# Optimization experiments

Hardware: AMD Instinct MI355X
Metric: run time of the kernel (lower is better)

## Reference

```python
import jax, jax.numpy as jnp
import numpy as np

NUM_HEADS = 16
EMBED_DIM = 1024
SEQ_LEN = 2048
BATCH = 2


def setup_inputs() -> dict:
    key = jax.random.key(0)
    ks = jax.random.split(key, 7)
    E = EMBED_DIM
    scale = 1.0 / np.sqrt(E)
    return {
        "query": jax.random.normal(ks[0], (SEQ_LEN, BATCH, E), jnp.float32),
        "key": jax.random.normal(ks[1], (SEQ_LEN, BATCH, E), jnp.float32),
        "value": jax.random.normal(ks[2], (SEQ_LEN, BATCH, E), jnp.float32),
        "in_proj_weight": jax.random.normal(ks[3], (3 * E, E), jnp.float32) * scale,
        "in_proj_bias": jnp.zeros((3 * E,), jnp.float32),
        "out_proj_weight": jax.random.normal(ks[4], (E, E), jnp.float32) * scale,
        "out_proj_bias": jnp.zeros((E,), jnp.float32),
    }


def reference(query, key, value, in_proj_weight, in_proj_bias, out_proj_weight, out_proj_bias):
    T, B, E = query.shape
    H = NUM_HEADS
    d = E // H
    scaling = float(d) ** -0.5
    # in-projections: rows [0:E) -> q, [E:2E) -> k, [2E:3E) -> v
    q = query @ in_proj_weight[:E].T + in_proj_bias[:E]
    k = key @ in_proj_weight[E:2 * E].T + in_proj_bias[E:2 * E]
    v = value @ in_proj_weight[2 * E:].T + in_proj_bias[2 * E:]
    q = q * scaling
    # (T, B, E) -> (B*H, T, d)
    q = q.reshape(T, B * H, d).transpose(1, 0, 2)
    k = k.reshape(T, B * H, d).transpose(1, 0, 2)
    v = v.reshape(T, B * H, d).transpose(1, 0, 2)
    S = k.shape[1]
    scores = jnp.einsum('ntd,nsd->nts', q, k)  # (B*H, T, S)
    attn = jax.nn.softmax(scores, axis=-1)
    out = jnp.einsum('nts,nsd->ntd', attn, v)  # (B*H, T, d)
    out = out.transpose(1, 0, 2).reshape(T, B, E)
    out = out @ out_proj_weight.T + out_proj_bias
    attn_avg = attn.reshape(B, H, T, S).sum(axis=1) / H
    return out, attn_avg
```

## Files before the change

kernel.cpp:

```cpp
#include <hip/hip_runtime.h>
#include <math.h>

#define T_LEN 2048
#define BATCH 2
#define EMB 1024
#define NHEAD 16
#define HDIM 64
#define BH (BATCH*NHEAD)
#define MROWS (T_LEN*BATCH)
#define QSCALE (0.125f * 1.4426950408889634f)
#define HEADBUF ((size_t)BH*T_LEN*HDIM)

typedef __attribute__((ext_vector_type(8))) short bf16x8;
typedef __attribute__((ext_vector_type(4))) float f32x4;

#define MFMA16(a,b,c) __builtin_amdgcn_mfma_f32_16x16x32_bf16(a,b,c,0,0,0)

__device__ __forceinline__ short f2bf(float f) {
    union { float f; unsigned u; } v; v.f = f;
    unsigned r = (v.u + 0x7FFFu + ((v.u >> 16) & 1u)) >> 16;
    return (short)(unsigned short)r;
}
__device__ __forceinline__ float bf2f(short s) {
    union { unsigned u; float f; } v; v.u = ((unsigned)(unsigned short)s) << 16;
    return v.f;
}
__device__ __forceinline__ unsigned cvtpk(float a, float b) {
    unsigned r;
    asm("v_cvt_pk_bf16_f32 %0, %1, %2" : "=v"(r) : "v"(a), "v"(b));
    return r;
}
__device__ __forceinline__ void gload16(const void* g, void* l) {
    __builtin_amdgcn_global_load_lds(
        (const __attribute__((address_space(1))) unsigned*)g,
        (__attribute__((address_space(3))) unsigned*)l, 16, 0, 0);
}

__global__ __launch_bounds__(256) void tobf16_kernel(
    const float* __restrict__ q, const float* __restrict__ k,
    const float* __restrict__ v, const float* __restrict__ w,
    const float* __restrict__ wo, short* __restrict__ out)
{
    size_t i8 = ((size_t)blockIdx.x * 256 + threadIdx.x) * 8;
    const float* src; size_t off;
    if (i8 < 12582912) {
        int sel = (int)(i8 >> 22);
        src = (sel == 0) ? q : (sel == 1) ? k : v;
        off = i8 & 4194303;
    } else if (i8 < 15728640) {
        src = w;  off = i8 - 12582912;
    } else {
        src = wo; off = i8 - 15728640;
    }
    float4 f0 = *(const float4*)(src + off);
    float4 f1 = *(const float4*)(src + off + 4);
    bf16x8 o;
    o[0]=f2bf(f0.x); o[1]=f2bf(f0.y); o[2]=f2bf(f0.z); o[3]=f2bf(f0.w);
    o[4]=f2bf(f1.x); o[5]=f2bf(f1.y); o[6]=f2bf(f1.z); o[7]=f2bf(f1.w);
    *(bf16x8*)(out + i8) = o;
}

__global__ __launch_bounds__(256) void inproj_gemm(
    const short* __restrict__ Xq, const short* __restrict__ Xk,
    const short* __restrict__ Xv, const short* __restrict__ Wb,
    const float* __restrict__ bias,
    short* __restrict__ qbuf, short* __restrict__ kbuf, short* __restrict__ vbuf)
{
    const int mBase = blockIdx.x * 128;
    const int nBase = blockIdx.y * 128;
    const int which = nBase >> 10;
    const short* __restrict__ X = (which == 0) ? Xq : (which == 1) ? Xk : Xv;
    short* __restrict__ dst = (which == 0) ? qbuf : (which == 1) ? kbuf : vbuf;

    __shared__ short Ast[128][64];
    __shared__ short Bst[128][64];

    const int tid  = threadIdx.x;
    const int lane = tid & 63;
    const int w    = tid >> 6;
    const int wr   = w >> 1, wc = w & 1;
    const int lr   = lane & 15, lg = lane >> 4;
    const int srow = tid >> 3;
    const int scol = (tid & 7) * 8;

    f32x4 acc[4][4] = {};

    for (int kb = 0; kb < EMB; kb += 64) {
        __syncthreads();
        #pragma unroll
        for (int j = 0; j < 4; ++j) {
            gload16(X  + (size_t)(mBase + j * 32 + srow) * EMB + kb + scol,
                    (char*)Ast + j * 4096 + w * 1024);
            gload16(Wb + (size_t)(nBase + j * 32 + srow) * EMB + kb + scol,
                    (char*)Bst + j * 4096 + w * 1024);
        }
        __syncthreads();
        #pragma unroll
        for (int ks = 0; ks < 2; ++ks) {
            bf16x8 af[4], bfr[4];
            #pragma unroll
            for (int rg = 0; rg < 4; ++rg)
                af[rg] = *(const bf16x8*)&Ast[wr * 64 + rg * 16 + lr][ks * 32 + lg * 8];
            #pragma unroll
            for (int cg = 0; cg < 4; ++cg)
                bfr[cg] = *(const bf16x8*)&Bst[wc * 64 + cg * 16 + lr][ks * 32 + lg * 8];
            #pragma unroll
            for (int rg = 0; rg < 4; ++rg)
                #pragma unroll
                for (int cg = 0; cg < 4; ++cg)
                    acc[rg][cg] = MFMA16(af[rg], bfr[cg], acc[rg][cg]);
        }
    }

    #pragma unroll
    for (int rg = 0; rg < 4; ++rg) {
        #pragma unroll
        for (int cg = 0; cg < 4; ++cg) {
            int n  = nBase + wc * 64 + cg * 16 + lr;
            int e  = n & 1023;
            int h  = e >> 6, dd = e & 63;
            float bs = bias[n];
            #pragma unroll
            for (int ri = 0; ri < 4; ++ri) {
                int m = mBase + wr * 64 + rg * 16 + lg * 4 + ri;
                int t = m >> 1, b = m & 1;
                float val = acc[rg][cg][ri] + bs;
                if (which == 0) val *= QSCALE;
                dst[((size_t)(b * NHEAD + h) * T_LEN + t) * HDIM + dd] = f2bf(val);
            }
        }
    }
}

__global__ __launch_bounds__(256) void flash_kernel(
    const short* __restrict__ qb, const short* __restrict__ kbuf,
    const short* __restrict__ vbuf, short* __restrict__ h1,
    short* __restrict__ h2, float* __restrict__ mlws)
{
    const int qt = blockIdx.x;
    const int hb = blockIdx.y;

    __shared__ short Kst[64][64];
    __shared__ short VT [64][64];
    __shared__ short Pst[64][72];

    const int tid  = threadIdx.x;
    const int lane = tid & 63;
    const int w    = tid >> 6;
    const int lr   = lane & 15, lg = lane >> 4;

    bf16x8 qa0, qa1;
    {
        const short* qsrc = qb + ((size_t)hb * T_LEN + qt * 64 + w * 16 + lr) * HDIM;
        qa0 = *(const bf16x8*)(qsrc + lg * 8);
        qa1 = *(const bf16x8*)(qsrc + 32 + lg * 8);
    }
    const int krow  = (lane >> 3);
    const int kc16  = (lane & 7) ^ krow;
    const int rb0 = ((0 + lg) ^ (lr & 7)) * 16;
    const int rb1 = ((4 + lg) ^ (lr & 7)) * 16;

    float m_r = -INFINITY, l_r = 0.f;
    f32x4 o_acc[4] = {};

    for (int st = 0; st < T_LEN / 64; ++st) {
        __syncthreads();
        #pragma unroll
        for (int it = 0; it < 2; ++it) {
            int r = (w * 2 + it) * 8 + krow;
            gload16(kbuf + ((size_t)hb * T_LEN + st * 64 + r) * HDIM + kc16 * 8,
                    (char*)Kst + (w * 2 + it) * 1024);
        }
        {
            int dc = tid & 7, s0 = (tid >> 3) * 2;
            const short* v0 = vbuf + ((size_t)hb * T_LEN + st * 64 + s0) * HDIM + dc * 8;
            bf16x8 va  = *(const bf16x8*)v0;
            bf16x8 vb2 = *(const bf16x8*)(v0 + HDIM);
            #pragma unroll
            for (int j = 0; j < 8; ++j) {
                int d = dc * 8 + j;
                unsigned pk = ((unsigned)(unsigned short)va[j]) |
                              (((unsigned)(unsigned short)vb2[j]) << 16);
                int byte = (d << 7) + (s0 << 1);
                byte ^= (((d & 7) ^ (d >> 3)) << 4);
                *(unsigned*)((char*)VT + byte) = pk;
            }
        }
        __syncthreads();

        f32x4 sc[4] = {};
        #pragma unroll
        for (int sg = 0; sg < 4; ++sg) {
            const char* krowp = (const char*)Kst + (sg * 16 + lr) * 128;
            bf16x8 kf0 = *(const bf16x8*)(krowp + rb0);
            bf16x8 kf1 = *(const bf16x8*)(krowp + rb1);
            sc[sg] = MFMA16(kf0, qa0, sc[sg]);
            sc[sg] = MFMA16(kf1, qa1, sc[sg]);
        }

        float mx = sc[0][0];
        #pragma unroll
        for (int sg = 0; sg < 4; ++sg)
            #pragma unroll
            for (int ri = 0; ri < 4; ++ri)
                mx = fmaxf(mx, sc[sg][ri]);
        mx = fmaxf(mx, __shfl_xor(mx, 16));
        mx = fmaxf(mx, __shfl_xor(mx, 32));
        if (__any(mx - m_r > 8.0f)) {
            float mnew = fmaxf(m_r, mx);
            float scl  = exp2f(m_r - mnew);
            l_r *= scl;
            m_r = mnew;
            float sclq[4];
            #pragma unroll
            for (int ri = 0; ri < 4; ++ri) sclq[ri] = __shfl(scl, lg * 20 + ri);
            #pragma unroll
            for (int dsub = 0; dsub < 4; ++dsub)
                #pragma unroll
                for (int ri = 0; ri < 4; ++ri)
                    o_acc[dsub][ri] *= sclq[ri];
        }
        float p[4][4], psum = 0.f;
        #pragma unroll
        for (int sg = 0; sg < 4; ++sg)
            #pragma unroll
            for (int ri = 0; ri < 4; ++ri) {
                p[sg][ri] = exp2f(sc[sg][ri] - m_r);
                psum += p[sg][ri];
            }
        psum += __shfl_xor(psum, 16);
        psum += __shfl_xor(psum, 32);
        l_r += psum;

        #pragma unroll
        for (int sg = 0; sg < 4; ++sg) {
            uint2 pk;
            pk.x = cvtpk(p[sg][0], p[sg][1]);
            pk.y = cvtpk(p[sg][2], p[sg][3]);
            *(uint2*)&Pst[w * 16 + lr][sg * 16 + lg * 4] = pk;
        }

        #pragma unroll
        for (int ks = 0; ks < 2; ++ks) {
            bf16x8 pa = *(const bf16x8*)&Pst[w * 16 + lr][ks * 32 + lg * 8];
            #pragma unroll
            for (int dsub = 0; dsub < 4; ++dsub) {
                int d = dsub * 16 + lr;
                int byte = (d << 7) + ((ks * 32 + lg * 8) << 1);
                byte ^= (((d & 7) ^ (d >> 3)) << 4);
                bf16x8 vf = *(const bf16x8*)((char*)VT + byte);
                o_acc[dsub] = MFMA16(pa, vf, o_acc[dsub]);
            }
        }
    }

    float inv = 1.0f / l_r;
    float invq[4];
    #pragma unroll
    for (int ri = 0; ri < 4; ++ri) invq[ri] = __shfl(inv, lg * 20 + ri);
    #pragma unroll
    for (int ri = 0; ri < 4; ++ri) {
        int row = qt * 64 + w * 16 + lg * 4 + ri;
        #pragma unroll
        for (int dsub = 0; dsub < 4; ++dsub) {
            float x = o_acc[dsub][ri] * invq[ri];
            size_t idx = ((size_t)hb * T_LEN + row) * HDIM + dsub * 16 + lr;
            short a = f2bf(x);
            h1[idx] = a;
            h2[idx] = f2bf(x - bf2f(a));
        }
    }
    if (lg == 0) {
        int row = qt * 64 + w * 16 + lr;
        mlws[(size_t)hb * T_LEN + row] = m_r + __log2f(l_r);
    }
}

__global__ __launch_bounds__(256) void avg_kernel(
    const short* __restrict__ qbuf, const short* __restrict__ kbuf,
    const float* __restrict__ mlws, float* __restrict__ attn_avg)
{
    const int st = blockIdx.x;
    const int qt = blockIdx.y;
    const int b  = blockIdx.z;

    __shared__ short K4[4][64][64];

    const int tid  = threadIdx.x;
    const int lane = tid & 63;
    const int w    = tid >> 6;
    const int lr   = lane & 15, lg = lane >> 4;

    f32x4 acc[4] = {};

    for (int rnd = 0; rnd < 4; ++rnd) {
        __syncthreads();
        #pragma unroll
        for (int hh = 0; hh < 4; ++hh) {
            int hb = b * NHEAD + rnd * 4 + hh;
            #pragma unroll
            for (int j = 0; j < 2; ++j) {
                int row = j * 32 + (tid >> 3);
                int col = (tid & 7) * 8;
                gload16(kbuf + ((size_t)hb * T_LEN + st * 64 + row) * HDIM + col,
                        (char*)K4[hh] + j * 4096 + w * 1024);
            }
        }
        __syncthreads();
        #pragma unroll
        for (int hh = 0; hh < 4; ++hh) {
            int hb = b * NHEAD + rnd * 4 + hh;
            const short* qsrc = qbuf + ((size_t)hb * T_LEN + qt * 64 + w * 16 + lr) * HDIM;
            bf16x8 qa0 = *(const bf16x8*)(qsrc + lg * 8);
            bf16x8 qa1 = *(const bf16x8*)(qsrc + 32 + lg * 8);

            f32x4 sc[4] = {};
            #pragma unroll
            for (int sg = 0; sg < 4; ++sg) {
                bf16x8 kf0 = *(const bf16x8*)&K4[hh][sg * 16 + lr][lg * 8];
                bf16x8 kf1 = *(const bf16x8*)&K4[hh][sg * 16 + lr][32 + lg * 8];
                sc[sg] = MFMA16(qa0, kf0, sc[sg]);
                sc[sg] = MFMA16(qa1, kf1, sc[sg]);
            }

            #pragma unroll
            for (int ri = 0; ri < 4; ++ri) {
                int row = qt * 64 + w * 16 + lg * 4 + ri;
                float ml = mlws[(size_t)hb * T_LEN + row];
                #pragma unroll
                for (int sg = 0; sg < 4; ++sg)
                    acc[sg][ri] += exp2f(sc[sg][ri] - ml);
            }
        }
    }

    const float invH = 1.0f / (float)NHEAD;
    #pragma unroll
    for (int ri = 0; ri < 4; ++ri) {
        int row = qt * 64 + w * 16 + lg * 4 + ri;
        #pragma unroll
        for (int sg = 0; sg < 4; ++sg)
            attn_avg[((size_t)b * T_LEN + row) * T_LEN + st * 64 + sg * 16 + lr] =
                acc[sg][ri] * invH;
    }
}

__global__ __launch_bounds__(256) void outproj_gemm(
    const short* __restrict__ h1, const short* __restrict__ h2,
    const short* __restrict__ Wob, const float* __restrict__ bo,
    float* __restrict__ out)
{
    const int mBase = blockIdx.x * 128;
    const int nBase = blockIdx.y * 128;

    __shared__ short A1st[128][64];
    __shared__ short A2st[128][64];
    __shared__ short Bst [128][64];

    const int tid  = threadIdx.x;
    const int lane = tid & 63;
    const int w    = tid >> 6;
    const int wr   = w >> 1, wc = w & 1;
    const int lr   = lane & 15, lg = lane >> 4;
    const int srow = tid >> 3;
    const int scol = (tid & 7) * 8;

    f32x4 acc[4][4] = {};

    for (int kb = 0; kb < EMB; kb += 64) {
        const int h = kb >> 6;
        __syncthreads();
        #pragma unroll
        for (int j = 0; j < 4; ++j) {
            int m = mBase + j * 32 + srow;
            int t = m >> 1, b = m & 1;
            size_t aoff = ((size_t)(b * NHEAD + h) * T_LEN + t) * HDIM + scol;
            gload16(h1 + aoff, (char*)A1st + j * 4096 + w * 1024);
            gload16(h2 + aoff, (char*)A2st + j * 4096 + w * 1024);
            gload16(Wob + (size_t)(nBase + j * 32 + srow) * EMB + kb + scol,
                    (char*)Bst + j * 4096 + w * 1024);
        }
        __syncthreads();
        #pragma unroll
        for (int ks = 0; ks < 2; ++ks) {
            bf16x8 a1[4], a2[4], bfr[4];
            #pragma unroll
            for (int rg = 0; rg < 4; ++rg) {
                a1[rg] = *(const bf16x8*)&A1st[wr * 64 + rg * 16 + lr][ks * 32 + lg * 8];
                a2[rg] = *(const bf16x8*)&A2st[wr * 64 + rg * 16 + lr][ks * 32 + lg * 8];
            }
            #pragma unroll
            for (int cg = 0; cg < 4; ++cg)
                bfr[cg] = *(const bf16x8*)&Bst[wc * 64 + cg * 16 + lr][ks * 32 + lg * 8];
            #pragma unroll
            for (int rg = 0; rg < 4; ++rg)
                #pragma unroll
                for (int cg = 0; cg < 4; ++cg) {
                    acc[rg][cg] = MFMA16(a1[rg], bfr[cg], acc[rg][cg]);
                    acc[rg][cg] = MFMA16(a2[rg], bfr[cg], acc[rg][cg]);
                }
        }
    }

    #pragma unroll
    for (int rg = 0; rg < 4; ++rg) {
        #pragma unroll
        for (int cg = 0; cg < 4; ++cg) {
            int n = nBase + wc * 64 + cg * 16 + lr;
            float bs = bo[n];
            #pragma unroll
            for (int ri = 0; ri < 4; ++ri) {
                int m = mBase + wr * 64 + rg * 16 + lg * 4 + ri;
                out[(size_t)m * EMB + n] = acc[rg][cg][ri] + bs;
            }
        }
    }
}

extern "C" void kernel_launch(void* const* d_in, const int* in_sizes, int n_in,
                              void* d_out, int out_size, void* d_ws, size_t ws_size,
                              hipStream_t stream)
{
    const float* query = (const float*)d_in[0];
    const float* key   = (const float*)d_in[1];
    const float* value = (const float*)d_in[2];
    const float* ipw   = (const float*)d_in[3];
    const float* ipb   = (const float*)d_in[4];
    const float* opw   = (const float*)d_in[5];
    const float* opb   = (const float*)d_in[6];

    short* qb  = (short*)d_ws;
    short* kb  = qb + HEADBUF;
    short* vb  = kb + HEADBUF;
    short* h1  = vb + HEADBUF;
    short* h2  = h1 + HEADBUF;
    short* xvb = h2 + HEADBUF;
    short* wbf = xvb + HEADBUF;
    short* wob = wbf + (size_t)3 * EMB * EMB;
    float* mlws = (float*)(wob + (size_t)EMB * EMB);

    float* out      = (float*)d_out;
    float* attn_avg = out + (size_t)MROWS * EMB;

    tobf16_kernel<<<8192, 256, 0, stream>>>(query, key, value, ipw, opw, h1);
    inproj_gemm  <<<dim3(MROWS / 128, 3 * EMB / 128), 256, 0, stream>>>(
        h1, h2, xvb, wbf, ipb, qb, kb, vb);
    flash_kernel <<<dim3(T_LEN / 64, BH),             256, 0, stream>>>(
        qb, kb, vb, h1, h2, mlws);
    avg_kernel   <<<dim3(T_LEN / 64, T_LEN / 64, BATCH), 256, 0, stream>>>(
        qb, kb, mlws, attn_avg);
    outproj_gemm <<<dim3(MROWS / 128, EMB / 128),     256, 0, stream>>>(
        h1, h2, wob, opb, out);
}
```

Baseline: 234.6 us.

## Store V pre-transposed and process 128 query rows per flash block

The in-projection GEMM now writes V in a head-major transposed layout (d by t), so the flash kernel can load V tiles into shared memory with the same async 16-byte loads and swizzle as K. This removes the per-tile register transpose and scattered LDS writes. Each flash block also handles 128 query rows (two 16-row fragments per wave), so each K/V tile is reused twice as much and the grid is halved. In exchange the V epilogue stores are strided by T_LEN, which may hurt write coalescing, and there are fewer blocks and more registers per thread, which may lower occupancy.

```diff
diff --git a/kernel.cpp b/kernel.cpp
--- a/kernel.cpp
+++ b/kernel.cpp
@@ -64,13 +64,12 @@
     const short* __restrict__ Xq, const short* __restrict__ Xk,
     const short* __restrict__ Xv, const short* __restrict__ Wb,
     const float* __restrict__ bias,
-    short* __restrict__ qbuf, short* __restrict__ kbuf, short* __restrict__ vbuf)
+    short* __restrict__ qbuf, short* __restrict__ kbuf, short* __restrict__ vbufT)
 {
     const int mBase = blockIdx.x * 128;
     const int nBase = blockIdx.y * 128;
     const int which = nBase >> 10;
     const short* __restrict__ X = (which == 0) ? Xq : (which == 1) ? Xk : Xv;
-    short* __restrict__ dst = (which == 0) ? qbuf : (which == 1) ? kbuf : vbuf;
 
     __shared__ short Ast[128][64];
     __shared__ short Bst[128][64];
@@ -125,8 +124,13 @@
                 int m = mBase + wr * 64 + rg * 16 + lg * 4 + ri;
                 int t = m >> 1, b = m & 1;
                 float val = acc[rg][cg][ri] + bs;
-                if (which == 0) val *= QSCALE;
-                dst[((size_t)(b * NHEAD + h) * T_LEN + t) * HDIM + dd] = f2bf(val);
+                short bfv;
+                if (which == 0) { bfv = f2bf(val * QSCALE);
+                    qbuf[((size_t)(b * NHEAD + h) * T_LEN + t) * HDIM + dd] = bfv; }
+                else if (which == 1) { bfv = f2bf(val);
+                    kbuf[((size_t)(b * NHEAD + h) * T_LEN + t) * HDIM + dd] = bfv; }
+                else { bfv = f2bf(val);
+                    vbufT[((size_t)(b * NHEAD + h) * HDIM + dd) * T_LEN + t] = bfv; }
             }
         }
     }
@@ -134,145 +138,149 @@
 
 __global__ __launch_bounds__(256) void flash_kernel(
     const short* __restrict__ qb, const short* __restrict__ kbuf,
-    const short* __restrict__ vbuf, short* __restrict__ h1,
+    const short* __restrict__ vbufT, short* __restrict__ h1,
     short* __restrict__ h2, float* __restrict__ mlws)
 {
     const int qt = blockIdx.x;
     const int hb = blockIdx.y;
 
     __shared__ short Kst[64][64];
-    __shared__ short VT [64][64];
-    __shared__ short Pst[64][72];
+    __shared__ short Vst[64][64];
+    __shared__ short Pst[128][72];
 
     const int tid  = threadIdx.x;
     const int lane = tid & 63;
     const int w    = tid >> 6;
     const int lr   = lane & 15, lg = lane >> 4;
 
-    bf16x8 qa0, qa1;
-    {
-        const short* qsrc = qb + ((size_t)hb * T_LEN + qt * 64 + w * 16 + lr) * HDIM;
-        qa0 = *(const bf16x8*)(qsrc + lg * 8);
-        qa1 = *(const bf16x8*)(qsrc + 32 + lg * 8);
-    }
-    const int krow  = (lane >> 3);
-    const int kc16  = (lane & 7) ^ krow;
+    bf16x8 qa[2][2];
+    #pragma unroll
+    for (int qf = 0; qf < 2; ++qf) {
+        const short* qsrc = qb + ((size_t)hb * T_LEN + qt * 128 + w * 32 + qf * 16 + lr) * HDIM;
+        qa[qf][0] = *(const bf16x8*)(qsrc + lg * 8);
+        qa[qf][1] = *(const bf16x8*)(qsrc + 32 + lg * 8);
+    }
+
+    const short* kbase = kbuf  + (size_t)hb * T_LEN * HDIM;
+    const short* vbase = vbufT + (size_t)hb * HDIM * T_LEN;
+
+    const int krow = lane >> 3;
+    const int kc16 = (lane & 7) ^ krow;
     const int rb0 = ((0 + lg) ^ (lr & 7)) * 16;
     const int rb1 = ((4 + lg) ^ (lr & 7)) * 16;
 
-    float m_r = -INFINITY, l_r = 0.f;
-    f32x4 o_acc[4] = {};
+    float m_r[2] = {-INFINITY, -INFINITY}, l_r[2] = {0.f, 0.f};
+    f32x4 o_acc[4][2] = {};
 
     for (int st = 0; st < T_LEN / 64; ++st) {
         __syncthreads();
         #pragma unroll
         for (int it = 0; it < 2; ++it) {
             int r = (w * 2 + it) * 8 + krow;
-            gload16(kbuf + ((size_t)hb * T_LEN + st * 64 + r) * HDIM + kc16 * 8,
+            gload16(kbase + (size_t)(st * 64 + r) * HDIM + kc16 * 8,
                     (char*)Kst + (w * 2 + it) * 1024);
-        }
-        {
-            int dc = tid & 7, s0 = (tid >> 3) * 2;
-            const short* v0 = vbuf + ((size_t)hb * T_LEN + st * 64 + s0) * HDIM + dc * 8;
-            bf16x8 va  = *(const bf16x8*)v0;
-            bf16x8 vb2 = *(const bf16x8*)(v0 + HDIM);
-            #pragma unroll
-            for (int j = 0; j < 8; ++j) {
-                int d = dc * 8 + j;
-                unsigned pk = ((unsigned)(unsigned short)va[j]) |
-                              (((unsigned)(unsigned short)vb2[j]) << 16);
-                int byte = (d << 7) + (s0 << 1);
-                byte ^= (((d & 7) ^ (d >> 3)) << 4);
-                *(unsigned*)((char*)VT + byte) = pk;
-            }
-        }
-        __syncthreads();
-
-        f32x4 sc[4] = {};
+            gload16(vbase + (size_t)r * T_LEN + st * 64 + kc16 * 8,
+                    (char*)Vst + (w * 2 + it) * 1024);
+        }
+        __syncthreads();
+
+        f32x4 sc[4][2] = {};
         #pragma unroll
         for (int sg = 0; sg < 4; ++sg) {
             const char* krowp = (const char*)Kst + (sg * 16 + lr) * 128;
             bf16x8 kf0 = *(const bf16x8*)(krowp + rb0);
             bf16x8 kf1 = *(const bf16x8*)(krowp + rb1);
-            sc[sg] = MFMA16(kf0, qa0, sc[sg]);
-            sc[sg] = MFMA16(kf1, qa1, sc[sg]);
-        }
-
-        float mx = sc[0][0];
-        #pragma unroll
-        for (int sg = 0; sg < 4; ++sg)
-            #pragma unroll
-            for (int ri = 0; ri < 4; ++ri)
-                mx = fmaxf(mx, sc[sg][ri]);
-        mx = fmaxf(mx, __shfl_xor(mx, 16));
-        mx = fmaxf(mx, __shfl_xor(mx, 32));
-        if (__any(mx - m_r > 8.0f)) {
-            float mnew = fmaxf(m_r, mx);
-            float scl  = exp2f(m_r - mnew);
-            l_r *= scl;
-            m_r = mnew;
-            float sclq[4];
-            #pragma unroll
-            for (int ri = 0; ri < 4; ++ri) sclq[ri] = __shfl(scl, lg * 20 + ri);
-            #pragma unroll
-            for (int dsub = 0; dsub < 4; ++dsub)
+            #pragma unroll
+            for (int qf = 0; qf < 2; ++qf) {
+                sc[sg][qf] = MFMA16(kf0, qa[qf][0], sc[sg][qf]);
+                sc[sg][qf] = MFMA16(kf1, qa[qf][1], sc[sg][qf]);
+            }
+        }
+
+        #pragma unroll
+        for (int qf = 0; qf < 2; ++qf) {
+            float mx = sc[0][qf][0];
+            #pragma unroll
+            for (int sg = 0; sg < 4; ++sg)
                 #pragma unroll
                 for (int ri = 0; ri < 4; ++ri)
-                    o_acc[dsub][ri] *= sclq[ri];
-        }
-        float p[4][4], psum = 0.f;
-        #pragma unroll
-        for (int sg = 0; sg < 4; ++sg)
-            #pragma unroll
-            for (int ri = 0; ri < 4; ++ri) {
-                p[sg][ri] = exp2f(sc[sg][ri] - m_r);
-                psum += p[sg][ri];
-            }
-        psum += __shfl_xor(psum, 16);
-        psum += __shfl_xor(psum, 32);
-        l_r += psum;
-
-        #pragma unroll
-        for (int sg = 0; sg < 4; ++sg) {
-            uint2 pk;
-            pk.x = cvtpk(p[sg][0], p[sg][1]);
-            pk.y = cvtpk(p[sg][2], p[sg][3]);
-            *(uint2*)&Pst[w * 16 + lr][sg * 16 + lg * 4] = pk;
+                    mx = fmaxf(mx, sc[sg][qf][ri]);
+            mx = fmaxf(mx, __shfl_xor(mx, 16));
+            mx = fmaxf(mx, __shfl_xor(mx, 32));
+            if (__any(mx - m_r[qf] > 8.0f)) {
+                float mnew = fmaxf(m_r[qf], mx);
+                float scl  = exp2f(m_r[qf] - mnew);
+                l_r[qf] *= scl;
+                m_r[qf] = mnew;
+                float sclq[4];
+                #pragma unroll
+                for (int ri = 0; ri < 4; ++ri) sclq[ri] = __shfl(scl, lg * 20 + ri);
+                #pragma unroll
+                for (int dsub = 0; dsub < 4; ++dsub)
+                    #pragma unroll
+                    for (int ri = 0; ri < 4; ++ri)
+                        o_acc[dsub][qf][ri] *= sclq[ri];
+            }
+            float p[4][4], psum = 0.f;
+            #pragma unroll
+            for (int sg = 0; sg < 4; ++sg)
+                #pragma unroll
+                for (int ri = 0; ri < 4; ++ri) {
+                    p[sg][ri] = exp2f(sc[sg][qf][ri] - m_r[qf]);
+                    psum += p[sg][ri];
+                }
+            psum += __shfl_xor(psum, 16);
+            psum += __shfl_xor(psum, 32);
+            l_r[qf] += psum;
+
+            #pragma unroll
+            for (int sg = 0; sg < 4; ++sg) {
+                uint2 pk;
+                pk.x = cvtpk(p[sg][0], p[sg][1]);
+                pk.y = cvtpk(p[sg][2], p[sg][3]);
+                *(uint2*)&Pst[w * 32 + qf * 16 + lr][sg * 16 + lg * 4] = pk;
+            }
         }
 
         #pragma unroll
         for (int ks = 0; ks < 2; ++ks) {
-            bf16x8 pa = *(const bf16x8*)&Pst[w * 16 + lr][ks * 32 + lg * 8];
+            bf16x8 pa[2];
+            #pragma unroll
+            for (int qf = 0; qf < 2; ++qf)
+                pa[qf] = *(const bf16x8*)&Pst[w * 32 + qf * 16 + lr][ks * 32 + lg * 8];
             #pragma unroll
             for (int dsub = 0; dsub < 4; ++dsub) {
-                int d = dsub * 16 + lr;
-                int byte = (d << 7) + ((ks * 32 + lg * 8) << 1);
-                byte ^= (((d & 7) ^ (d >> 3)) << 4);
-                bf16x8 vf = *(const bf16x8*)((char*)VT + byte);
-                o_acc[dsub] = MFMA16(pa, vf, o_acc[dsub]);
-            }
-        }
-    }
-
-    float inv = 1.0f / l_r;
-    float invq[4];
+                const char* vrowp = (const char*)Vst + (dsub * 16 + lr) * 128;
+                bf16x8 vf = *(const bf16x8*)(vrowp + (ks ? rb1 : rb0));
+                #pragma unroll
+                for (int qf = 0; qf < 2; ++qf)
+                    o_acc[dsub][qf] = MFMA16(pa[qf], vf, o_acc[dsub][qf]);
+            }
+        }
+    }
+
     #pragma unroll
-    for (int ri = 0; ri < 4; ++ri) invq[ri] = __shfl(inv, lg * 20 + ri);
-    #pragma unroll
-    for (int ri = 0; ri < 4; ++ri) {
-        int row = qt * 64 + w * 16 + lg * 4 + ri;
-        #pragma unroll
-        for (int dsub = 0; dsub < 4; ++dsub) {
-            float x = o_acc[dsub][ri] * invq[ri];
-            size_t idx = ((size_t)hb * T_LEN + row) * HDIM + dsub * 16 + lr;
-            short a = f2bf(x);
-            h1[idx] = a;
-            h2[idx] = f2bf(x - bf2f(a));
-        }
-    }
-    if (lg == 0) {
-        int row = qt * 64 + w * 16 + lr;
-        mlws[(size_t)hb * T_LEN + row] = m_r + __log2f(l_r);
+    for (int qf = 0; qf < 2; ++qf) {
+        float inv = 1.0f / l_r[qf];
+        float invq[4];
+        #pragma unroll
+        for (int ri = 0; ri < 4; ++ri) invq[ri] = __shfl(inv, lg * 20 + ri);
+        #pragma unroll
+        for (int ri = 0; ri < 4; ++ri) {
+            int row = qt * 128 + w * 32 + qf * 16 + lg * 4 + ri;
+            #pragma unroll
+            for (int dsub = 0; dsub < 4; ++dsub) {
+                float x = o_acc[dsub][qf][ri] * invq[ri];
+                size_t idx = ((size_t)hb * T_LEN + row) * HDIM + dsub * 16 + lr;
+                short a = f2bf(x);
+                h1[idx] = a;
+                h2[idx] = f2bf(x - bf2f(a));
+            }
+        }
+        if (lg == 0) {
+            int row = qt * 128 + w * 32 + qf * 16 + lr;
+            mlws[(size_t)hb * T_LEN + row] = m_r[qf] + __log2f(l_r[qf]);
+        }
     }
 }
 
@@ -431,8 +439,8 @@
 
     short* qb  = (short*)d_ws;
     short* kb  = qb + HEADBUF;
-    short* vb  = kb + HEADBUF;
-    short* h1  = vb + HEADBUF;
+    short* vbT = kb + HEADBUF;
+    short* h1  = vbT + HEADBUF;
     short* h2  = h1 + HEADBUF;
     short* xvb = h2 + HEADBUF;
     short* wbf = xvb + HEADBUF;
@@ -444,9 +452,9 @@
 
     tobf16_kernel<<<8192, 256, 0, stream>>>(query, key, value, ipw, opw, h1);
     inproj_gemm  <<<dim3(MROWS / 128, 3 * EMB / 128), 256, 0, stream>>>(
-        h1, h2, xvb, wbf, ipb, qb, kb, vb);
-    flash_kernel <<<dim3(T_LEN / 64, BH),             256, 0, stream>>>(
-        qb, kb, vb, h1, h2, mlws);
+        h1, h2, xvb, wbf, ipb, qb, kb, vbT);
+    flash_kernel <<<dim3(T_LEN / 128, BH),            256, 0, stream>>>(
+        qb, kb, vbT, h1, h2, mlws);
     avg_kernel   <<<dim3(T_LEN / 64, T_LEN / 64, BATCH), 256, 0, stream>>>(
         qb, kb, mlws, attn_avg);
     outproj_gemm <<<dim3(MROWS / 128, EMB / 128),     256, 0, stream>>>(
```

New measurement: 241.6 us. +3.0%, slower.

## Store V transposed, double-buffer K/V tiles in flash and avg kernels

Applied to the files above, without the earlier changes.

The in-projection GEMM now writes V transposed per head (d-major), so the flash kernel can load V tiles with async 16-byte global-to-LDS loads instead of a register transpose. Both the flash and avg kernels double-buffer their LDS tiles and prefetch the next tile while computing the current one, which removes one barrier per iteration. The row-sum shuffle reduction is deferred until after the loop. Risks: the transposed V store in the GEMM epilogue is strided and poorly coalesced, and the extra LDS per block may reduce occupancy.

```diff
diff --git a/kernel.cpp b/kernel.cpp
--- a/kernel.cpp
+++ b/kernel.cpp
@@ -64,13 +64,12 @@
     const short* __restrict__ Xq, const short* __restrict__ Xk,
     const short* __restrict__ Xv, const short* __restrict__ Wb,
     const float* __restrict__ bias,
-    short* __restrict__ qbuf, short* __restrict__ kbuf, short* __restrict__ vbuf)
+    short* __restrict__ qbuf, short* __restrict__ kbuf, short* __restrict__ vbufT)
 {
     const int mBase = blockIdx.x * 128;
     const int nBase = blockIdx.y * 128;
     const int which = nBase >> 10;
     const short* __restrict__ X = (which == 0) ? Xq : (which == 1) ? Xk : Xv;
-    short* __restrict__ dst = (which == 0) ? qbuf : (which == 1) ? kbuf : vbuf;
 
     __shared__ short Ast[128][64];
     __shared__ short Bst[128][64];
@@ -125,8 +124,13 @@
                 int m = mBase + wr * 64 + rg * 16 + lg * 4 + ri;
                 int t = m >> 1, b = m & 1;
                 float val = acc[rg][cg][ri] + bs;
-                if (which == 0) val *= QSCALE;
-                dst[((size_t)(b * NHEAD + h) * T_LEN + t) * HDIM + dd] = f2bf(val);
+                short bfv;
+                if (which == 0) { bfv = f2bf(val * QSCALE);
+                    qbuf[((size_t)(b * NHEAD + h) * T_LEN + t) * HDIM + dd] = bfv; }
+                else if (which == 1) { bfv = f2bf(val);
+                    kbuf[((size_t)(b * NHEAD + h) * T_LEN + t) * HDIM + dd] = bfv; }
+                else { bfv = f2bf(val);
+                    vbufT[((size_t)(b * NHEAD + h) * HDIM + dd) * T_LEN + t] = bfv; }
             }
         }
     }
@@ -134,14 +138,14 @@
 
 __global__ __launch_bounds__(256) void flash_kernel(
     const short* __restrict__ qb, const short* __restrict__ kbuf,
-    const short* __restrict__ vbuf, short* __restrict__ h1,
+    const short* __restrict__ vbufT, short* __restrict__ h1,
     short* __restrict__ h2, float* __restrict__ mlws)
 {
     const int qt = blockIdx.x;
     const int hb = blockIdx.y;
 
-    __shared__ short Kst[64][64];
-    __shared__ short VT [64][64];
+    __shared__ short Kst[2][64][64];
+    __shared__ short Vst[2][64][64];
     __shared__ short Pst[64][72];
 
     const int tid  = threadIdx.x;
@@ -155,43 +159,45 @@
         qa0 = *(const bf16x8*)(qsrc + lg * 8);
         qa1 = *(const bf16x8*)(qsrc + 32 + lg * 8);
     }
-    const int krow  = (lane >> 3);
-    const int kc16  = (lane & 7) ^ krow;
+
+    const short* kbase = kbuf  + (size_t)hb * T_LEN * HDIM;
+    const short* vbase = vbufT + (size_t)hb * HDIM * T_LEN;
+
+    const int krow = lane >> 3;
+    const int kc16 = (lane & 7) ^ krow;
     const int rb0 = ((0 + lg) ^ (lr & 7)) * 16;
     const int rb1 = ((4 + lg) ^ (lr & 7)) * 16;
 
     float m_r = -INFINITY, l_r = 0.f;
     f32x4 o_acc[4] = {};
 
+    #pragma unroll
+    for (int it = 0; it < 2; ++it) {
+        int r = (w * 2 + it) * 8 + krow;
+        gload16(kbase + (size_t)r * HDIM + kc16 * 8,
+                (char*)Kst[0] + (w * 2 + it) * 1024);
+        gload16(vbase + (size_t)r * T_LEN + kc16 * 8,
+                (char*)Vst[0] + (w * 2 + it) * 1024);
+    }
+    __syncthreads();
+
+    int cur = 0;
     for (int st = 0; st < T_LEN / 64; ++st) {
-        __syncthreads();
-        #pragma unroll
-        for (int it = 0; it < 2; ++it) {
-            int r = (w * 2 + it) * 8 + krow;
-            gload16(kbuf + ((size_t)hb * T_LEN + st * 64 + r) * HDIM + kc16 * 8,
-                    (char*)Kst + (w * 2 + it) * 1024);
-        }
-        {
-            int dc = tid & 7, s0 = (tid >> 3) * 2;
-            const short* v0 = vbuf + ((size_t)hb * T_LEN + st * 64 + s0) * HDIM + dc * 8;
-            bf16x8 va  = *(const bf16x8*)v0;
-            bf16x8 vb2 = *(const bf16x8*)(v0 + HDIM);
-            #pragma unroll
-            for (int j = 0; j < 8; ++j) {
-                int d = dc * 8 + j;
-                unsigned pk = ((unsigned)(unsigned short)va[j]) |
-                              (((unsigned)(unsigned short)vb2[j]) << 16);
-                int byte = (d << 7) + (s0 << 1);
-                byte ^= (((d & 7) ^ (d >> 3)) << 4);
-                *(unsigned*)((char*)VT + byte) = pk;
-            }
-        }
-        __syncthreads();
+        if (st + 1 < T_LEN / 64) {
+            #pragma unroll
+            for (int it = 0; it < 2; ++it) {
+                int r = (w * 2 + it) * 8 + krow;
+                gload16(kbase + (size_t)((st + 1) * 64 + r) * HDIM + kc16 * 8,
+                        (char*)Kst[cur ^ 1] + (w * 2 + it) * 1024);
+                gload16(vbase + (size_t)r * T_LEN + (st + 1) * 64 + kc16 * 8,
+                        (char*)Vst[cur ^ 1] + (w * 2 + it) * 1024);
+            }
+        }
 
         f32x4 sc[4] = {};
         #pragma unroll
         for (int sg = 0; sg < 4; ++sg) {
-            const char* krowp = (const char*)Kst + (sg * 16 + lr) * 128;
+            const char* krowp = (const char*)Kst[cur] + (sg * 16 + lr) * 128;
             bf16x8 kf0 = *(const bf16x8*)(krowp + rb0);
             bf16x8 kf1 = *(const bf16x8*)(krowp + rb1);
             sc[sg] = MFMA16(kf0, qa0, sc[sg]);
@@ -220,17 +226,14 @@
                 for (int ri = 0; ri < 4; ++ri)
                     o_acc[dsub][ri] *= sclq[ri];
         }
-        float p[4][4], psum = 0.f;
+        float p[4][4];
         #pragma unroll
         for (int sg = 0; sg < 4; ++sg)
             #pragma unroll
             for (int ri = 0; ri < 4; ++ri) {
                 p[sg][ri] = exp2f(sc[sg][ri] - m_r);
-                psum += p[sg][ri];
-            }
-        psum += __shfl_xor(psum, 16);
-        psum += __shfl_xor(psum, 32);
-        l_r += psum;
+                l_r += p[sg][ri];
+            }
 
         #pragma unroll
         for (int sg = 0; sg < 4; ++sg) {
@@ -245,16 +248,20 @@
             bf16x8 pa = *(const bf16x8*)&Pst[w * 16 + lr][ks * 32 + lg * 8];
             #pragma unroll
             for (int dsub = 0; dsub < 4; ++dsub) {
-                int d = dsub * 16 + lr;
-                int byte = (d << 7) + ((ks * 32 + lg * 8) << 1);
-                byte ^= (((d & 7) ^ (d >> 3)) << 4);
-                bf16x8 vf = *(const bf16x8*)((char*)VT + byte);
+                const char* vrowp = (const char*)Vst[cur] + (dsub * 16 + lr) * 128;
+                bf16x8 vf = *(const bf16x8*)(vrowp + (ks ? rb1 : rb0));
                 o_acc[dsub] = MFMA16(pa, vf, o_acc[dsub]);
             }
         }
-    }
-
-    float inv = 1.0f / l_r;
+
+        __syncthreads();
+        cur ^= 1;
+    }
+
+    float lsum = l_r;
+    lsum += __shfl_xor(lsum, 16);
+    lsum += __shfl_xor(lsum, 32);
+    float inv = 1.0f / lsum;
     float invq[4];
     #pragma unroll
     for (int ri = 0; ri < 4; ++ri) invq[ri] = __shfl(inv, lg * 20 + ri);
@@ -272,7 +279,7 @@
     }
     if (lg == 0) {
         int row = qt * 64 + w * 16 + lr;
-        mlws[(size_t)hb * T_LEN + row] = m_r + __log2f(l_r);
+        mlws[(size_t)hb * T_LEN + row] = m_r + __log2f(lsum);
     }
 }
 
@@ -284,32 +291,42 @@
     const int qt = blockIdx.y;
     const int b  = blockIdx.z;
 
-    __shared__ short K4[4][64][64];
+    __shared__ short K2[2][2][64][64];
 
     const int tid  = threadIdx.x;
     const int lane = tid & 63;
     const int w    = tid >> 6;
     const int lr   = lane & 15, lg = lane >> 4;
+    const int srow = tid >> 3;
+    const int scol = (tid & 7) * 8;
 
     f32x4 acc[4] = {};
 
-    for (int rnd = 0; rnd < 4; ++rnd) {
-        __syncthreads();
-        #pragma unroll
-        for (int hh = 0; hh < 4; ++hh) {
-            int hb = b * NHEAD + rnd * 4 + hh;
-            #pragma unroll
-            for (int j = 0; j < 2; ++j) {
-                int row = j * 32 + (tid >> 3);
-                int col = (tid & 7) * 8;
-                gload16(kbuf + ((size_t)hb * T_LEN + st * 64 + row) * HDIM + col,
-                        (char*)K4[hh] + j * 4096 + w * 1024);
-            }
-        }
-        __syncthreads();
-        #pragma unroll
-        for (int hh = 0; hh < 4; ++hh) {
-            int hb = b * NHEAD + rnd * 4 + hh;
+    #pragma unroll
+    for (int hh = 0; hh < 2; ++hh) {
+        int hb0 = b * NHEAD + hh;
+        #pragma unroll
+        for (int j = 0; j < 2; ++j)
+            gload16(kbuf + ((size_t)hb0 * T_LEN + st * 64 + j * 32 + srow) * HDIM + scol,
+                    (char*)K2[0][hh] + j * 4096 + w * 1024);
+    }
+    __syncthreads();
+
+    int cur = 0;
+    for (int rnd = 0; rnd < 8; ++rnd) {
+        if (rnd + 1 < 8) {
+            #pragma unroll
+            for (int hh = 0; hh < 2; ++hh) {
+                int hbn = b * NHEAD + (rnd + 1) * 2 + hh;
+                #pragma unroll
+                for (int j = 0; j < 2; ++j)
+                    gload16(kbuf + ((size_t)hbn * T_LEN + st * 64 + j * 32 + srow) * HDIM + scol,
+                            (char*)K2[cur ^ 1][hh] + j * 4096 + w * 1024);
+            }
+        }
+        #pragma unroll
+        for (int hh = 0; hh < 2; ++hh) {
+            int hb = b * NHEAD + rnd * 2 + hh;
             const short* qsrc = qbuf + ((size_t)hb * T_LEN + qt * 64 + w * 16 + lr) * HDIM;
             bf16x8 qa0 = *(const bf16x8*)(qsrc + lg * 8);
             bf16x8 qa1 = *(const bf16x8*)(qsrc + 32 + lg * 8);
@@ -317,8 +334,8 @@
             f32x4 sc[4] = {};
             #pragma unroll
             for (int sg = 0; sg < 4; ++sg) {
-                bf16x8 kf0 = *(const bf16x8*)&K4[hh][sg * 16 + lr][lg * 8];
-                bf16x8 kf1 = *(const bf16x8*)&K4[hh][sg * 16 + lr][32 + lg * 8];
+                bf16x8 kf0 = *(const bf16x8*)&K2[cur][hh][sg * 16 + lr][lg * 8];
+                bf16x8 kf1 = *(const bf16x8*)&K2[cur][hh][sg * 16 + lr][32 + lg * 8];
                 sc[sg] = MFMA16(qa0, kf0, sc[sg]);
                 sc[sg] = MFMA16(qa1, kf1, sc[sg]);
             }
@@ -332,6 +349,8 @@
                     acc[sg][ri] += exp2f(sc[sg][ri] - ml);
             }
         }
+        __syncthreads();
+        cur ^= 1;
     }
 
     const float invH = 1.0f / (float)NHEAD;
@@ -431,8 +450,8 @@
 
     short* qb  = (short*)d_ws;
     short* kb  = qb + HEADBUF;
-    short* vb  = kb + HEADBUF;
-    short* h1  = vb + HEADBUF;
+    short* vbT = kb + HEADBUF;
+    short* h1  = vbT + HEADBUF;
     short* h2  = h1 + HEADBUF;
     short* xvb = h2 + HEADBUF;
     short* wbf = xvb + HEADBUF;
@@ -444,9 +463,9 @@
 
     tobf16_kernel<<<8192, 256, 0, stream>>>(query, key, value, ipw, opw, h1);
     inproj_gemm  <<<dim3(MROWS / 128, 3 * EMB / 128), 256, 0, stream>>>(
-        h1, h2, xvb, wbf, ipb, qb, kb, vb);
+        h1, h2, xvb, wbf, ipb, qb, kb, vbT);
     flash_kernel <<<dim3(T_LEN / 64, BH),             256, 0, stream>>>(
-        qb, kb, vb, h1, h2, mlws);
+        qb, kb, vbT, h1, h2, mlws);
     avg_kernel   <<<dim3(T_LEN / 64, T_LEN / 64, BATCH), 256, 0, stream>>>(
         qb, kb, mlws, attn_avg);
     outproj_gemm <<<dim3(MROWS / 128, EMB / 128),     256, 0, stream>>>(
```

Result: slower. 249.4 us (+6.3%).
